# Kernel tuning notes

Measured on AMD Instinct MI355X. Metric: run time of the kernel, lower is better.

## Reference

```python
import jax, jax.numpy as jnp
import numpy as np

B, S, D_IN, D_OUT = 2, 2048, 4096, 4096
E, K, R = 8, 2, 16
SCALING = 32.0 / 16.0  # lora_alpha / r (use_rslora=False)


def setup_inputs() -> dict:
    key = jax.random.key(0)
    ks = jax.random.split(key, 6)
    x = jax.random.normal(ks[0], (B, S, D_IN), dtype=jnp.float32)
    gate_w = jax.random.normal(ks[1], (E, D_IN), dtype=jnp.float32) * 0.02
    base_w = jax.random.normal(ks[2], (D_OUT, D_IN), dtype=jnp.float32) * 0.02
    base_b = jax.random.normal(ks[3], (D_OUT,), dtype=jnp.float32) * 0.02
    lora_A = jax.random.normal(ks[4], (E, R, D_IN), dtype=jnp.float32) * 0.02
    lora_B = jax.random.normal(ks[5], (E, D_OUT, R), dtype=jnp.float32) * 0.02
    return {"x": x, "gate_w": gate_w, "base_w": base_w, "base_b": base_b,
            "lora_A": lora_A, "lora_B": lora_B}


def reference(x, gate_w, base_w, base_b, lora_A, lora_B):
    # gate + top-k routing
    gate_logits = jnp.einsum('bsd,ed->bse', x, gate_w)           # [B,S,E]
    weights, selected = jax.lax.top_k(gate_logits, K)            # [B,S,K]
    weights = jax.nn.softmax(weights.astype(jnp.float32), axis=2).astype(x.dtype)
    # base linear
    result = jnp.einsum('bsd,od->bso', x, base_w) + base_b       # [B,S,O]
    # scatter routing weights into a dense per-expert weight map [B,S,E]
    w_full = jnp.sum(jax.nn.one_hot(selected, E, dtype=x.dtype) * weights[..., None], axis=2)
    # low-rank LoRA for every expert (tiny r), combine weighted per token
    low = jnp.einsum('bsd,erd->ebsr', x, lora_A)                 # [E,B,S,R]
    lora_out = jnp.einsum('ebsr,eor,bse->bso', low, lora_B, w_full)
    result = result + SCALING * lora_out
    return result
```

## Files before the change

kernel.cpp:

```cpp
#include <hip/hip_runtime.h>
#include <hip/hip_bf16.h>

typedef unsigned short u16;
typedef __bf16  bf16x8 __attribute__((ext_vector_type(8)));
typedef float   f32x4  __attribute__((ext_vector_type(4)));

#define T_TOK 4096
#define DIN   4096
#define DOUT  4096
#define NEXP  8
#define ER    128
#define SPLIT 8
#define KCH   (DIN / SPLIT)

#define OFF_XB    0u
#define OFF_WB    33554432u
#define OFF_AB    67108864u
#define OFF_BS2   68157440u
#define OFF_U     69206016u
#define OFF_BBF   70254592u
#define OFF_LG    70270976u
#define OFF_GPART 70402048u

__device__ __forceinline__ void async16(void* lds, const void* g) {
    __builtin_amdgcn_global_load_lds(
        (const __attribute__((address_space(1))) void*)g,
        (__attribute__((address_space(3))) void*)lds,
        16, 0, 0);
}

static __device__ __forceinline__ u16 f2b(float f) {
    __hip_bfloat16 h = __float2bfloat16(f);
    return *(u16*)&h;
}

__device__ __forceinline__ bf16x8 lds8(const u16* base, int row, int grp) {
    return *(const bf16x8*)((const char*)base + row * 128 + (((grp ^ row) & 7) * 16));
}

#define FENCE() asm volatile("" ::: "memory")
#define RAW_BAR() do { FENCE(); __builtin_amdgcn_s_barrier(); FENCE(); } while (0)
#define LGKM0() do { asm volatile("s_waitcnt lgkmcnt(0)" ::: "memory"); \
                     __builtin_amdgcn_sched_barrier(0); } while (0)
#define WAITV(N) do { asm volatile("s_waitcnt vmcnt(" #N ")" ::: "memory"); \
                      __builtin_amdgcn_sched_barrier(0); } while (0)

__global__ __launch_bounds__(256) void prep_x(const float* __restrict__ x,
                                              const float* __restrict__ gw,
                                              u16* __restrict__ xb,
                                              float* __restrict__ Lg) {
    const int w = threadIdx.x >> 6, lid = threadIdx.x & 63;
    const int t0 = (blockIdx.x * 4 + w) * 4;
    float acc[4][8];
#pragma unroll
    for (int j = 0; j < 4; ++j)
#pragma unroll
        for (int e = 0; e < 8; ++e) acc[j][e] = 0.f;
    for (int i = lid; i < DIN / 4; i += 64) {
        float4 gv[8];
#pragma unroll
        for (int e = 0; e < 8; ++e)
            gv[e] = ((const float4*)(gw + (size_t)e * DIN))[i];
#pragma unroll
        for (int j = 0; j < 4; ++j) {
            float4 xv = ((const float4*)(x + (size_t)(t0 + j) * DIN))[i];
            ushort4 o = { f2b(xv.x), f2b(xv.y), f2b(xv.z), f2b(xv.w) };
            ((ushort4*)(xb + (size_t)(t0 + j) * DIN))[i] = o;
#pragma unroll
            for (int e = 0; e < 8; ++e)
                acc[j][e] += xv.x * gv[e].x + xv.y * gv[e].y + xv.z * gv[e].z + xv.w * gv[e].w;
        }
    }
#pragma unroll
    for (int j = 0; j < 4; ++j)
#pragma unroll
        for (int e = 0; e < 8; ++e) {
            float v = acc[j][e];
            for (int off = 32; off; off >>= 1) v += __shfl_down(v, off, 64);
            if (lid == 0) Lg[(t0 + j) * 8 + e] = v;
        }
}

__global__ __launch_bounds__(256) void convert_w_pack(const float* __restrict__ wsrc,
                                                      const float* __restrict__ lora_A,
                                                      const float* __restrict__ lora_B,
                                                      const float* __restrict__ base_b,
                                                      uint4* __restrict__ wb,
                                                      u16* __restrict__ ab,
                                                      u16* __restrict__ bs2,
                                                      float* __restrict__ bbf) {
    const int bid = blockIdx.x;
    if (bid < 8192) {
        int li = bid * 256 + threadIdx.x;
        const float4* s = (const float4*)wsrc;
        float4 a = s[2 * li], b = s[2 * li + 1];
        uint4 o;
        o.x = (unsigned)f2b(a.x) | ((unsigned)f2b(a.y) << 16);
        o.y = (unsigned)f2b(a.z) | ((unsigned)f2b(a.w) << 16);
        o.z = (unsigned)f2b(b.x) | ((unsigned)f2b(b.y) << 16);
        o.w = (unsigned)f2b(b.z) | ((unsigned)f2b(b.w) << 16);
        wb[li] = o;
    } else {
        int idx = (bid - 8192) * 256 + threadIdx.x;
        if (idx < 524288) {
            ab[idx] = f2b(lora_A[idx]);
        } else if (idx < 1048576) {
            int j = idx - 524288;
            int o = j >> 7, c = j & 127, e = c >> 4, r = c & 15;
            bs2[j] = f2b(lora_B[(e * DOUT + o) * 16 + r] * 2.0f);
        } else if (idx < 1052672) {
            int j = idx - 1048576;
            bbf[j] = base_b[j];
        }
    }
}

__global__ __launch_bounds__(256) void gemm1(const u16* __restrict__ X,
                                             const u16* __restrict__ ab,
                                             float* __restrict__ Gpart) {
    __shared__ __align__(16) u16 As[128 * 64];
    __shared__ __align__(16) u16 Bs[128 * 64];
    const int mb = blockIdx.x, s = blockIdx.y;
    const int w = threadIdx.x >> 6, lid = threadIdx.x & 63;
    const int lrow = lid >> 3;
    const int lcolb = ((lid & 7) ^ lrow) * 16;

    f32x4 acc[2][8];
#pragma unroll
    for (int i = 0; i < 2; ++i)
#pragma unroll
        for (int j = 0; j < 8; ++j) acc[i][j] = (f32x4){0.f, 0.f, 0.f, 0.f};

    int k0 = s * KCH;
    for (int kt = 0; kt < KCH / 64; ++kt, k0 += 64) {
#pragma unroll
        for (int q = 0; q < 4; ++q) {
            int c = w * 4 + q;
            int arow = mb * 128 + c * 8 + lrow;
            async16((char*)As + c * 1024,
                    (const char*)X + ((size_t)arow * DIN + k0) * 2 + lcolb);
            async16((char*)Bs + c * 1024,
                    (const char*)ab + ((size_t)(c * 8 + lrow) * DIN + k0) * 2 + lcolb);
        }
        __syncthreads();
        const int quad = lid >> 4, half = lid & 15;
#pragma unroll
        for (int ks8 = 0; ks8 < 8; ks8 += 4) {
            bf16x8 a[2], b[8];
#pragma unroll
            for (int i = 0; i < 2; ++i)
                a[i] = lds8(As, w * 32 + i * 16 + half, ks8 + quad);
#pragma unroll
            for (int j = 0; j < 8; ++j)
                b[j] = lds8(Bs, j * 16 + half, ks8 + quad);
#pragma unroll
            for (int i = 0; i < 2; ++i)
#pragma unroll
                for (int j = 0; j < 8; ++j)
                    acc[i][j] = __builtin_amdgcn_mfma_f32_16x16x32_bf16(a[i], b[j], acc[i][j], 0, 0, 0);
        }
        __syncthreads();
    }
    const int quad = lid >> 4, nl = lid & 15;
#pragma unroll
    for (int i = 0; i < 2; ++i)
#pragma unroll
        for (int j = 0; j < 8; ++j) {
            int n = j * 16 + nl;
            int t = mb * 128 + w * 32 + i * 16 + quad * 4;
            float* dst = Gpart + ((size_t)s * T_TOK + t) * ER + n;
#pragma unroll
            for (int r = 0; r < 4; ++r) dst[(size_t)r * ER] = acc[i][j][r];
        }
}

__global__ __launch_bounds__(256) void route_u(const float* __restrict__ Gpart,
                                               const float* __restrict__ Lg,
                                               u16* __restrict__ U) {
    __shared__ float wmap[16][9];
    const int t0 = blockIdx.x * 16;
    const int tid = threadIdx.x;
    if (tid < 16) {
        float l[8];
#pragma unroll
        for (int e = 0; e < 8; ++e) l[e] = Lg[(t0 + tid) * 8 + e];
        int e1 = 0; float b1 = l[0];
#pragma unroll
        for (int e = 1; e < 8; ++e) if (l[e] > b1) { b1 = l[e]; e1 = e; }
        int e2 = -1; float b2 = -3.4e38f;
#pragma unroll
        for (int e = 0; e < 8; ++e) if (e != e1 && l[e] > b2) { b2 = l[e]; e2 = e; }
        float ex = __expf(b2 - b1);
        float inv = 1.f / (1.f + ex);
#pragma unroll
        for (int e = 0; e < 8; ++e) wmap[tid][e] = 0.f;
        wmap[tid][e1] = inv;
        wmap[tid][e2] = ex * inv;
    }
    __syncthreads();
#pragma unroll
    for (int it = 0; it < 2; ++it) {
        int idx = it * 256 + tid;
        int tl = idx >> 5, c4 = idx & 31;
        float4 s = {0.f, 0.f, 0.f, 0.f};
        for (int sp = 0; sp < SPLIT; ++sp) {
            float4 g = ((const float4*)(Gpart + ((size_t)sp * T_TOK + t0 + tl) * ER))[c4];
            s.x += g.x; s.y += g.y; s.z += g.z; s.w += g.w;
        }
        float wv = wmap[tl][c4 >> 2];
        ushort4 o = { f2b(s.x * wv), f2b(s.y * wv), f2b(s.z * wv), f2b(s.w * wv) };
        ((ushort4*)(U + (size_t)(t0 + tl) * ER))[c4] = o;
    }
}

__global__ __launch_bounds__(512) void gemm2(const u16* __restrict__ X,
                                             const u16* __restrict__ W,
                                             const float* __restrict__ bbf,
                                             const u16* __restrict__ U,
                                             const u16* __restrict__ Bs2,
                                             float* __restrict__ out) {
    extern __shared__ __align__(16) char smem[];
    const int tid = threadIdx.x;
    const int l = tid & 63, w = tid >> 6;
    const int wm = w & 1, wn = w >> 1;

    const int bid = blockIdx.x;
    const int sw = (bid & 7) * 32 + (bid >> 3);
    const int mb = sw >> 4, nb = sw & 15;

    const int srow = w * 16 + (l >> 2);
    const int gcol = (((l & 3) ^ ((l >> 3) & 3)) << 3);
    const int ldso = w * 1024;

    const int hl = l & 15, quad = l >> 4;
    const int sgr = ((quad ^ ((hl >> 1) & 3)) << 4);
    const int rbA = (wm * 128 + hl) * 64 + sgr;
    const int rbB = (wn * 64 + hl) * 64 + sgr;

    const u16* xrow = X   + (size_t)(mb * 256 + srow) * DIN;
    const u16* wrw  = W   + (size_t)(nb * 256 + srow) * DIN;
    const u16* urow = U   + (size_t)(mb * 256 + srow) * ER;
    const u16* brow = Bs2 + (size_t)(nb * 256 + srow) * ER;

    f32x4 acc[8][4];
#pragma unroll
    for (int i = 0; i < 8; ++i)
#pragma unroll
        for (int j = 0; j < 4; ++j) acc[i][j] = (f32x4){0.f, 0.f, 0.f, 0.f};

    auto stageA = [&](int t2, int ks) {
        char* dst = smem + ((t2 & 1) << 16) + (ks << 14) + ldso;
        if (t2 < 64) {
            const int col = t2 * 64 + ks * 32 + gcol;
            async16(dst,        xrow + col);
            async16(dst + 8192, xrow + (size_t)128 * DIN + col);
        } else {
            const int col = (t2 - 64) * 64 + ks * 32 + gcol;
            async16(dst,        urow + col);
            async16(dst + 8192, urow + 128 * ER + col);
        }
    };
    auto stageB = [&](int t2, int ks) {
        char* dst = smem + ((t2 & 1) << 16) + 32768 + (ks << 14) + ldso;
        if (t2 < 64) {
            const int col = t2 * 64 + ks * 32 + gcol;
            async16(dst,        wrw + col);
            async16(dst + 8192, wrw + (size_t)128 * DIN + col);
        } else {
            const int col = (t2 - 64) * 64 + ks * 32 + gcol;
            async16(dst,        brow + col);
            async16(dst + 8192, brow + 128 * ER + col);
        }
    };

    bf16x8 bfr[4];

#define PHASE(SEG, KS, IB, READB, STAGE, WV) do {                              \
        const char* rs_ = (SEG) + ((KS) << 14);                                \
        bf16x8 a_[4];                                                          \
        _Pragma("unroll")                                                      \
        for (int i_ = 0; i_ < 4; ++i_)                                         \
            a_[i_] = *(const bf16x8*)(rs_ + rbA + ((IB) + i_) * 1024);         \
        if (READB) {                                                           \
            _Pragma("unroll")                                                  \
            for (int j_ = 0; j_ < 4; ++j_)                                     \
                bfr[j_] = *(const bf16x8*)(rs_ + 32768 + rbB + j_ * 1024);     \
        }                                                                      \
        STAGE;                                                                 \
        WV;                                                                    \
        RAW_BAR();                                                             \
        LGKM0();                                                               \
        __builtin_amdgcn_s_setprio(1);                                         \
        _Pragma("unroll")                                                      \
        for (int i_ = 0; i_ < 4; ++i_)                                         \
            _Pragma("unroll")                                                  \
            for (int j_ = 0; j_ < 4; ++j_)                                     \
                acc[(IB) + i_][j_] = __builtin_amdgcn_mfma_f32_16x16x32_bf16(  \
                    a_[i_], bfr[j_], acc[(IB) + i_][j_], 0, 0, 0);             \
        __builtin_amdgcn_s_setprio(0);                                         \
        RAW_BAR();                                                             \
    } while (0)

    stageA(0, 0); stageB(0, 0); stageA(0, 1); stageB(0, 1);
    stageA(1, 0); stageB(1, 0);
    WAITV(8);
    RAW_BAR();

#pragma unroll 1
    for (int t = 0; t < 64; ++t) {
        const char* seg = smem + ((t & 1) << 16);
        PHASE(seg, 0, 0, true,  { stageA(t + 1, 1); }, {});
        PHASE(seg, 0, 4, false, { stageB(t + 1, 1); }, { WAITV(8); });
        PHASE(seg, 1, 0, true,  { stageA(t + 2, 0); }, {});
        PHASE(seg, 1, 4, false, { stageB(t + 2, 0); }, { WAITV(8); });
    }
    {
        const char* seg = smem;
        PHASE(seg, 0, 0, true,  { stageA(65, 1); }, {});
        PHASE(seg, 0, 4, false, { stageB(65, 1); }, { WAITV(8); });
        PHASE(seg, 1, 0, true,  {}, {});
        PHASE(seg, 1, 4, false, {}, { WAITV(4); });
    }
    {
        const char* seg = smem + 65536;
        PHASE(seg, 0, 0, true,  {}, {});
        PHASE(seg, 0, 4, false, {}, { WAITV(0); });
        PHASE(seg, 1, 0, true,  {}, {});
        PHASE(seg, 1, 4, false, {}, {});
    }
#undef PHASE

    const int nl = hl;
#pragma unroll
    for (int j = 0; j < 4; ++j) {
        const int n = nb * 256 + wn * 64 + j * 16 + nl;
        const float bz = bbf[n];
#pragma unroll
        for (int i = 0; i < 8; ++i) {
            const int m = mb * 256 + wm * 128 + i * 16 + quad * 4;
            float* dst = out + (size_t)m * DOUT + n;
#pragma unroll
            for (int r = 0; r < 4; ++r)
                dst[(size_t)r * DOUT] = acc[i][j][r] + bz;
        }
    }
}

extern "C" void kernel_launch(void* const* d_in, const int* in_sizes, int n_in,
                              void* d_out, int out_size, void* d_ws, size_t ws_size,
                              hipStream_t stream) {
    const float* x      = (const float*)d_in[0];
    const float* gate_w = (const float*)d_in[1];
    const float* base_w = (const float*)d_in[2];
    const float* base_b = (const float*)d_in[3];
    const float* lora_A = (const float*)d_in[4];
    const float* lora_B = (const float*)d_in[5];
    float* out = (float*)d_out;

    char* ws = (char*)d_ws;
    u16*   xb    = (u16*)(ws + OFF_XB);
    u16*   wb    = (u16*)(ws + OFF_WB);
    u16*   ab    = (u16*)(ws + OFF_AB);
    u16*   bs2   = (u16*)(ws + OFF_BS2);
    u16*   U     = (u16*)(ws + OFF_U);
    float* bbf   = (float*)(ws + OFF_BBF);
    float* Lg    = (float*)(ws + OFF_LG);
    float* Gpart = (float*)(ws + OFF_GPART);

    static bool attr_done = false;
    if (!attr_done) {
        (void)hipFuncSetAttribute(reinterpret_cast<const void*>(gemm2),
                                  hipFuncAttributeMaxDynamicSharedMemorySize, 131072);
        attr_done = true;
    }

    prep_x<<<T_TOK / 16, 256, 0, stream>>>(x, gate_w, xb, Lg);
    convert_w_pack<<<8192 + 4112, 256, 0, stream>>>(base_w, lora_A, lora_B, base_b,
                                                    (uint4*)wb, ab, bs2, bbf);
    gemm1<<<dim3(32, SPLIT), 256, 0, stream>>>(xb, ab, Gpart);
    route_u<<<T_TOK / 16, 256, 0, stream>>>(Gpart, Lg, U);
    gemm2<<<256, 512, 131072, stream>>>(xb, wb, bbf, U, bs2, out);
}
```

Baseline: 334.2 us.

## Merge prep kernels into one launch and drop trailing barrier in gemm2 phases

Result: faster. 317.3 us (-5.0%).

```diff
diff --git a/kernel.cpp b/kernel.cpp
--- a/kernel.cpp
+++ b/kernel.cpp
@@ -45,53 +45,52 @@
 #define WAITV(N) do { asm volatile("s_waitcnt vmcnt(" #N ")" ::: "memory"); \
                       __builtin_amdgcn_sched_barrier(0); } while (0)
 
-__global__ __launch_bounds__(256) void prep_x(const float* __restrict__ x,
-                                              const float* __restrict__ gw,
-                                              u16* __restrict__ xb,
-                                              float* __restrict__ Lg) {
-    const int w = threadIdx.x >> 6, lid = threadIdx.x & 63;
-    const int t0 = (blockIdx.x * 4 + w) * 4;
-    float acc[4][8];
-#pragma unroll
-    for (int j = 0; j < 4; ++j)
-#pragma unroll
-        for (int e = 0; e < 8; ++e) acc[j][e] = 0.f;
-    for (int i = lid; i < DIN / 4; i += 64) {
-        float4 gv[8];
-#pragma unroll
-        for (int e = 0; e < 8; ++e)
-            gv[e] = ((const float4*)(gw + (size_t)e * DIN))[i];
-#pragma unroll
-        for (int j = 0; j < 4; ++j) {
-            float4 xv = ((const float4*)(x + (size_t)(t0 + j) * DIN))[i];
-            ushort4 o = { f2b(xv.x), f2b(xv.y), f2b(xv.z), f2b(xv.w) };
-            ((ushort4*)(xb + (size_t)(t0 + j) * DIN))[i] = o;
+__global__ __launch_bounds__(256) void prep_all(const float* __restrict__ x,
+                                                const float* __restrict__ gw,
+                                                const float* __restrict__ wsrc,
+                                                const float* __restrict__ lora_A,
+                                                const float* __restrict__ lora_B,
+                                                const float* __restrict__ base_b,
+                                                u16* __restrict__ xb,
+                                                float* __restrict__ Lg,
+                                                uint4* __restrict__ wb,
+                                                u16* __restrict__ ab,
+                                                u16* __restrict__ bs2,
+                                                float* __restrict__ bbf) {
+    const int bid = blockIdx.x;
+    if (bid < 512) {
+        const int w = threadIdx.x >> 6, lid = threadIdx.x & 63;
+        const int t0 = (bid * 4 + w) * 2;
+        float acc[2][8];
+#pragma unroll
+        for (int j = 0; j < 2; ++j)
+#pragma unroll
+            for (int e = 0; e < 8; ++e) acc[j][e] = 0.f;
+        for (int i = lid; i < DIN / 4; i += 64) {
+            float4 gv[8];
 #pragma unroll
             for (int e = 0; e < 8; ++e)
-                acc[j][e] += xv.x * gv[e].x + xv.y * gv[e].y + xv.z * gv[e].z + xv.w * gv[e].w;
-        }
-    }
-#pragma unroll
-    for (int j = 0; j < 4; ++j)
-#pragma unroll
-        for (int e = 0; e < 8; ++e) {
-            float v = acc[j][e];
-            for (int off = 32; off; off >>= 1) v += __shfl_down(v, off, 64);
-            if (lid == 0) Lg[(t0 + j) * 8 + e] = v;
-        }
-}
-
-__global__ __launch_bounds__(256) void convert_w_pack(const float* __restrict__ wsrc,
-                                                      const float* __restrict__ lora_A,
-                                                      const float* __restrict__ lora_B,
-                                                      const float* __restrict__ base_b,
-                                                      uint4* __restrict__ wb,
-                                                      u16* __restrict__ ab,
-                                                      u16* __restrict__ bs2,
-                                                      float* __restrict__ bbf) {
-    const int bid = blockIdx.x;
-    if (bid < 8192) {
-        int li = bid * 256 + threadIdx.x;
+                gv[e] = ((const float4*)(gw + (size_t)e * DIN))[i];
+#pragma unroll
+            for (int j = 0; j < 2; ++j) {
+                float4 xv = ((const float4*)(x + (size_t)(t0 + j) * DIN))[i];
+                ushort4 o = { f2b(xv.x), f2b(xv.y), f2b(xv.z), f2b(xv.w) };
+                ((ushort4*)(xb + (size_t)(t0 + j) * DIN))[i] = o;
+#pragma unroll
+                for (int e = 0; e < 8; ++e)
+                    acc[j][e] += xv.x * gv[e].x + xv.y * gv[e].y + xv.z * gv[e].z + xv.w * gv[e].w;
+            }
+        }
+#pragma unroll
+        for (int j = 0; j < 2; ++j)
+#pragma unroll
+            for (int e = 0; e < 8; ++e) {
+                float v = acc[j][e];
+                for (int off = 32; off; off >>= 1) v += __shfl_down(v, off, 64);
+                if (lid == 0) Lg[(t0 + j) * 8 + e] = v;
+            }
+    } else if (bid < 8704) {
+        int li = (bid - 512) * 256 + threadIdx.x;
         const float4* s = (const float4*)wsrc;
         float4 a = s[2 * li], b = s[2 * li + 1];
         uint4 o;
@@ -101,7 +100,7 @@
         o.w = (unsigned)f2b(b.z) | ((unsigned)f2b(b.w) << 16);
         wb[li] = o;
     } else {
-        int idx = (bid - 8192) * 256 + threadIdx.x;
+        int idx = (bid - 8704) * 256 + threadIdx.x;
         if (idx < 524288) {
             ab[idx] = f2b(lora_A[idx]);
         } else if (idx < 1048576) {
@@ -298,26 +297,27 @@
                 acc[(IB) + i_][j_] = __builtin_amdgcn_mfma_f32_16x16x32_bf16(  \
                     a_[i_], bfr[j_], acc[(IB) + i_][j_], 0, 0, 0);             \
         __builtin_amdgcn_s_setprio(0);                                         \
-        RAW_BAR();                                                             \
+        __builtin_amdgcn_sched_barrier(0);                                     \
     } while (0)
 
-    stageA(0, 0); stageB(0, 0); stageA(0, 1); stageB(0, 1);
-    stageA(1, 0); stageB(1, 0);
+    stageA(0, 0); stageB(0, 0);
+    stageA(0, 1); stageB(0, 1);
+    stageB(1, 0); stageA(1, 0);
     WAITV(8);
     RAW_BAR();
 
 #pragma unroll 1
     for (int t = 0; t < 64; ++t) {
         const char* seg = smem + ((t & 1) << 16);
-        PHASE(seg, 0, 0, true,  { stageA(t + 1, 1); }, {});
-        PHASE(seg, 0, 4, false, { stageB(t + 1, 1); }, { WAITV(8); });
-        PHASE(seg, 1, 0, true,  { stageA(t + 2, 0); }, {});
-        PHASE(seg, 1, 4, false, { stageB(t + 2, 0); }, { WAITV(8); });
+        PHASE(seg, 0, 0, true,  { stageB(t + 1, 1); }, {});
+        PHASE(seg, 0, 4, false, { stageA(t + 1, 1); }, { WAITV(8); });
+        PHASE(seg, 1, 0, true,  { stageB(t + 2, 0); }, {});
+        PHASE(seg, 1, 4, false, { stageA(t + 2, 0); }, { WAITV(8); });
     }
     {
         const char* seg = smem;
-        PHASE(seg, 0, 0, true,  { stageA(65, 1); }, {});
-        PHASE(seg, 0, 4, false, { stageB(65, 1); }, { WAITV(8); });
+        PHASE(seg, 0, 0, true,  { stageB(65, 1); }, {});
+        PHASE(seg, 0, 4, false, { stageA(65, 1); }, { WAITV(8); });
         PHASE(seg, 1, 0, true,  {}, {});
         PHASE(seg, 1, 4, false, {}, { WAITV(4); });
     }
@@ -374,9 +374,8 @@
         attr_done = true;
     }
 
-    prep_x<<<T_TOK / 16, 256, 0, stream>>>(x, gate_w, xb, Lg);
-    convert_w_pack<<<8192 + 4112, 256, 0, stream>>>(base_w, lora_A, lora_B, base_b,
-                                                    (uint4*)wb, ab, bs2, bbf);
+    prep_all<<<12816, 256, 0, stream>>>(x, gate_w, base_w, lora_A, lora_B, base_b,
+                                        xb, Lg, (uint4*)wb, ab, bs2, bbf);
     gemm1<<<dim3(32, SPLIT), 256, 0, stream>>>(xb, ab, Gpart);
     route_u<<<T_TOK / 16, 256, 0, stream>>>(Gpart, Lg, U);
     gemm2<<<256, 512, 131072, stream>>>(xb, wb, bbf, U, bs2, out);
```
